# Kernel optimization log

Measured on AMD Instinct MI355X. Metric: run time of the kernel, lower is better.

## Reference

```python
import jax, jax.numpy as jnp
import numpy as np

EPS = 1e-6

def _phi(x):
    # ELU + 1 feature map: strictly positive
    return jax.nn.elu(x) + 1.0

def setup_inputs() -> dict:
    key = jax.random.key(0)
    kq, kk, kv = jax.random.split(key, 3)
    B, T, H, D = 4, 8192, 16, 64
    q = jax.random.normal(kq, (B, T, H, D), dtype=jnp.float32)
    k = jax.random.normal(kk, (B, T, H, D), dtype=jnp.float32)
    v = jax.random.normal(kv, (B, T, H, D), dtype=jnp.float32)
    return {"q": q, "k": k, "v": v}

def _linear_attention(q, k, v):
    # q,k,v: [B,T,H,D] -> out [B,T,H,D]
    phi_q = _phi(q)
    phi_k = _phi(k)
    # time-major for scan: [T,B,H,D]
    pq = jnp.moveaxis(phi_q, 1, 0)
    pk = jnp.moveaxis(phi_k, 1, 0)
    vv = jnp.moveaxis(v, 1, 0)
    B, H, D = pq.shape[1], pq.shape[2], pq.shape[3]
    S0 = jnp.zeros((B, H, D, D), dtype=q.dtype)
    z0 = jnp.zeros((B, H, D), dtype=q.dtype)

    def step(carry, inp):
        S, z = carry
        q_t, k_t, v_t = inp  # each [B,H,D]
        S = S + k_t[..., :, None] * v_t[..., None, :]  # [B,H,D,D]
        z = z + k_t
        num = jnp.einsum('bhd,bhde->bhe', q_t, S)
        den = jnp.einsum('bhd,bhd->bh', q_t, z) + EPS
        return (S, z), num / den[..., None]

    _, out = jax.lax.scan(step, (S0, z0), (pq, pk, vv))
    return jnp.moveaxis(out, 0, 1)  # [B,T,H,D]

def reference(q, k, v):
    return _linear_attention(q, k, v)
```

## Files before the change

kernel.cpp:

```cpp
#include <hip/hip_runtime.h>
#include <hip/hip_bf16.h>


#define EPS_ 1e-6f

constexpr int Bc  = 4;
constexpr int Tc  = 8192;
constexpr int Hc  = 16;
constexpr int Dc  = 64;
constexpr int CH  = 128;
constexpr int NCH = Tc / CH;
constexpr int BHc = Bc * Hc;
constexpr int REC = Dc * Dc + Dc;

typedef short  bf16x8 __attribute__((ext_vector_type(8)));
typedef float  f32x4  __attribute__((ext_vector_type(4)));

__device__ __forceinline__ float phi_f(float x) {
    return x > 0.f ? x + 1.f : __expf(x);
}
__device__ __forceinline__ unsigned short f2b(float x) {
    __hip_bfloat16 b = __float2bfloat16(x);
    return __builtin_bit_cast(unsigned short, b);
}
__device__ __forceinline__ float b2f(unsigned short u) {
    return __uint_as_float(((unsigned)u) << 16);
}

__global__ __launch_bounds__(256) void k_chunksum(const float* __restrict__ kin,
                                                  const float* __restrict__ vin,
                                                  float* __restrict__ ws) {
    const int chunk = blockIdx.x;
    const int bh = chunk >> 6, c = chunk & (NCH - 1);
    const int b  = bh >> 4,    h = bh & 15;
    const int t0 = c * CH;
    const int tid = threadIdx.x;

    __shared__ unsigned short ktr[64][136];
    __shared__ unsigned short vtr[64][136];
    __shared__ float zred[4][64];

    {
        const int c0 = (tid & 15) << 2;
        const int rl = ((tid >> 4) & 15) << 2;
        #pragma unroll
        for (int sh = 0; sh < 2; ++sh) {
            const int r0 = rl + sh * 64;
            unsigned short hk[4][4], hv[4][4];
            #pragma unroll
            for (int jj = 0; jj < 4; ++jj) {
                const size_t g = ((((size_t)b * Tc) + (t0 + r0 + jj)) * Hc + h) * Dc + c0;
                const float4 kk = *(const float4*)(kin + g);
                const float4 vv = *(const float4*)(vin + g);
                hk[jj][0] = f2b(phi_f(kk.x)); hk[jj][1] = f2b(phi_f(kk.y));
                hk[jj][2] = f2b(phi_f(kk.z)); hk[jj][3] = f2b(phi_f(kk.w));
                hv[jj][0] = f2b(vv.x); hv[jj][1] = f2b(vv.y);
                hv[jj][2] = f2b(vv.z); hv[jj][3] = f2b(vv.w);
            }
            #pragma unroll
            for (int j = 0; j < 4; ++j) {
                *(ushort4*)&ktr[c0 + j][r0] = make_ushort4(hk[0][j], hk[1][j], hk[2][j], hk[3][j]);
                *(ushort4*)&vtr[c0 + j][r0] = make_ushort4(hv[0][j], hv[1][j], hv[2][j], hv[3][j]);
            }
        }
    }
    __syncthreads();

    {
        const int d = tid & 63, part = tid >> 6;
        float zs = 0.f;
        #pragma unroll
        for (int j = 0; j < 4; j++) {
            bf16x8 kv = *(const bf16x8*)&ktr[d][part * 32 + j * 8];
            #pragma unroll
            for (int u = 0; u < 8; u++) zs += b2f((unsigned short)kv[u]);
        }
        zred[part][d] = zs;
    }

    const int w = tid >> 6, lane = tid & 63;
    const int l15 = lane & 15, quad = lane >> 4;
    f32x4 acc[4];
    #pragma unroll
    for (int nt = 0; nt < 4; nt++) acc[nt] = (f32x4){0.f, 0.f, 0.f, 0.f};
    #pragma unroll
    for (int ks = 0; ks < 4; ks++) {
        bf16x8 a = *(const bf16x8*)&vtr[16 * w + l15][quad * 8 + ks * 32];
        #pragma unroll
        for (int nt = 0; nt < 4; nt++) {
            bf16x8 bb = *(const bf16x8*)&ktr[16 * nt + l15][quad * 8 + ks * 32];
            acc[nt] = __builtin_amdgcn_mfma_f32_16x16x32_bf16(a, bb, acc[nt], 0, 0, 0);
        }
    }
    __syncthreads();

    float* rec = ws + (size_t)chunk * REC;
    #pragma unroll
    for (int nt = 0; nt < 4; nt++)
        #pragma unroll
        for (int r = 0; r < 4; r++) {
            const int e = 16 * w + quad * 4 + r;
            const int d = 16 * nt + l15;
            rec[e * 64 + d] = acc[nt][r];
        }
    if (tid < 64)
        rec[4096 + tid] = zred[0][tid] + zred[1][tid] + zred[2][tid] + zred[3][tid];
}

__global__ __launch_bounds__(256) void k_prefix(float* __restrict__ ws) {
    const int bh = blockIdx.x;
    const int e  = blockIdx.y * 256 + threadIdx.x;
    if (e >= REC) return;
    float* p = ws + (size_t)bh * NCH * REC + e;
    float run = 0.f;
    #pragma unroll 4
    for (int c = 0; c < NCH; ++c) {
        float x = p[(size_t)c * REC];
        p[(size_t)c * REC] = run;
        run += x;
    }
}

__global__ __launch_bounds__(512, 4) void k_output(const float* __restrict__ qin,
                                                   const float* __restrict__ kin,
                                                   const float* __restrict__ vin,
                                                   const float* __restrict__ ws,
                                                   float* __restrict__ outp) {
    const int chunk = blockIdx.x;
    const int bh = chunk >> 6, c = chunk & (NCH - 1);
    const int b = bh >> 4, h = bh & 15;
    const int t0 = c * CH;
    const int tid = threadIdx.x;
    const int w = tid >> 6, lane = tid & 63;
    const int l15 = lane & 15, quad = lane >> 4;

    __shared__ unsigned short qb[128][72];
    __shared__ unsigned short kb[128][72];
    __shared__ unsigned short sb[64][72];
    __shared__ unsigned short vb[64][136];
    __shared__ float zsh[64];
    __shared__ float den[128];

    {
        const int row = tid >> 2, cb = (tid & 3) << 4;
        const size_t g = ((((size_t)b * Tc) + (t0 + row)) * Hc + h) * Dc + cb;
        const float4* qp = (const float4*)(qin + g);
        const float4* kp = (const float4*)(kin + g);
        #pragma unroll
        for (int i = 0; i < 4; i++) {
            float4 qq = qp[i];
            float4 kk = kp[i];
            *(ushort4*)&qb[row][cb + 4 * i] =
                make_ushort4(f2b(phi_f(qq.x)), f2b(phi_f(qq.y)), f2b(phi_f(qq.z)), f2b(phi_f(qq.w)));
            *(ushort4*)&kb[row][cb + 4 * i] =
                make_ushort4(f2b(phi_f(kk.x)), f2b(phi_f(kk.y)), f2b(phi_f(kk.z)), f2b(phi_f(kk.w)));
        }
    }
    {
        const int c0 = (tid & 15) << 2;
        const int r0 = (tid >> 4) << 2;
        unsigned short hv[4][4];
        #pragma unroll
        for (int jj = 0; jj < 4; ++jj) {
            const size_t g = ((((size_t)b * Tc) + (t0 + r0 + jj)) * Hc + h) * Dc + c0;
            const float4 vv = *(const float4*)(vin + g);
            hv[jj][0] = f2b(vv.x); hv[jj][1] = f2b(vv.y);
            hv[jj][2] = f2b(vv.z); hv[jj][3] = f2b(vv.w);
        }
        #pragma unroll
        for (int j = 0; j < 4; ++j)
            *(ushort4*)&vb[c0 + j][r0] = make_ushort4(hv[0][j], hv[1][j], hv[2][j], hv[3][j]);
    }
    {
        const float* rec = ws + (size_t)chunk * REC;
        #pragma unroll
        for (int i = 0; i < 2; i++) {
            const int idx = tid + i * 512;
            float4 sv = ((const float4*)rec)[idx];
            const int flat = idx * 4, e = flat >> 6, d = flat & 63;
            *(ushort4*)&sb[e][d] = make_ushort4(f2b(sv.x), f2b(sv.y), f2b(sv.z), f2b(sv.w));
        }
        if (tid < 16) {
            float4 zv = ((const float4*)(rec + 4096))[tid];
            zsh[tid * 4 + 0] = zv.x; zsh[tid * 4 + 1] = zv.y;
            zsh[tid * 4 + 2] = zv.z; zsh[tid * 4 + 3] = zv.w;
        }
    }
    __syncthreads();

    if (tid < 128) {
        float s = 0.f;
        #pragma unroll
        for (int j = 0; j < 8; j++) {
            bf16x8 qv = *(const bf16x8*)&qb[tid][j * 8];
            #pragma unroll
            for (int u = 0; u < 8; u++) s += b2f((unsigned short)qv[u]) * zsh[j * 8 + u];
        }
        den[tid] = s + EPS_;
    }

    f32x4 acc[4];
    #pragma unroll
    for (int nt = 0; nt < 4; nt++) acc[nt] = (f32x4){0.f, 0.f, 0.f, 0.f};
    #pragma unroll
    for (int ks = 0; ks < 2; ks++) {
        bf16x8 a = *(const bf16x8*)&qb[16 * w + l15][quad * 8 + ks * 32];
        #pragma unroll
        for (int nt = 0; nt < 4; nt++) {
            bf16x8 bb = *(const bf16x8*)&sb[16 * nt + l15][quad * 8 + ks * 32];
            acc[nt] = __builtin_amdgcn_mfma_f32_16x16x32_bf16(a, bb, acc[nt], 0, 0, 0);
        }
    }

    f32x4 wt[8];
    #pragma unroll
    for (int nt = 0; nt < 8; nt++) wt[nt] = (f32x4){0.f, 0.f, 0.f, 0.f};
    #pragma unroll
    for (int ks = 0; ks < 2; ks++) {
        bf16x8 a = *(const bf16x8*)&qb[16 * w + l15][quad * 8 + ks * 32];
        #pragma unroll
        for (int nt = 0; nt < 4; nt++) {
            bf16x8 bb = *(const bf16x8*)&kb[16 * nt + l15][quad * 8 + ks * 32];
            wt[nt] = __builtin_amdgcn_mfma_f32_16x16x32_bf16(a, bb, wt[nt], 0, 0, 0);
        }
        if (w >= 4) {
            #pragma unroll
            for (int nt = 4; nt < 8; nt++) {
                bf16x8 bb = *(const bf16x8*)&kb[16 * nt + l15][quad * 8 + ks * 32];
                wt[nt] = __builtin_amdgcn_mfma_f32_16x16x32_bf16(a, bb, wt[nt], 0, 0, 0);
            }
        }
    }
    __syncthreads();

    {
        const int tbase = 16 * w + quad * 4;
        float rsum[4] = {0.f, 0.f, 0.f, 0.f};
        #pragma unroll
        for (int nt = 0; nt < 4; nt++) {
            const int s = 16 * nt + l15;
            #pragma unroll
            for (int r = 0; r < 4; r++) {
                float val = (s > tbase + r) ? 0.f : wt[nt][r];
                unsigned short wb16 = f2b(val);
                kb[tbase + r][s] = wb16;
                rsum[r] += b2f(wb16);
            }
        }
        if (w >= 4) {
            #pragma unroll
            for (int nt = 4; nt < 8; nt++) {
                const int s = 16 * nt + l15;
                #pragma unroll
                for (int r = 0; r < 4; r++) {
                    float val = (s > tbase + r) ? 0.f : wt[nt][r];
                    unsigned short wb16 = f2b(val);
                    qb[tbase + r][s - 64] = wb16;
                    rsum[r] += b2f(wb16);
                }
            }
        }
        #pragma unroll
        for (int r = 0; r < 4; r++) {
            float rs = rsum[r];
            rs += __shfl_xor(rs, 8, 16);
            rs += __shfl_xor(rs, 4, 16);
            rs += __shfl_xor(rs, 2, 16);
            rs += __shfl_xor(rs, 1, 16);
            if (l15 == 0) den[tbase + r] += rs;
        }
    }
    __syncthreads();

    #pragma unroll
    for (int ks = 0; ks < 2; ks++) {
        bf16x8 a = *(const bf16x8*)&kb[16 * w + l15][quad * 8 + ks * 32];
        #pragma unroll
        for (int nt = 0; nt < 4; nt++) {
            bf16x8 bb = *(const bf16x8*)&vb[16 * nt + l15][quad * 8 + ks * 32];
            acc[nt] = __builtin_amdgcn_mfma_f32_16x16x32_bf16(a, bb, acc[nt], 0, 0, 0);
        }
    }
    if (w >= 4) {
        #pragma unroll
        for (int ks = 2; ks < 4; ks++) {
            bf16x8 a = *(const bf16x8*)&qb[16 * w + l15][quad * 8 + (ks - 2) * 32];
            #pragma unroll
            for (int nt = 0; nt < 4; nt++) {
                bf16x8 bb = *(const bf16x8*)&vb[16 * nt + l15][quad * 8 + ks * 32];
                acc[nt] = __builtin_amdgcn_mfma_f32_16x16x32_bf16(a, bb, acc[nt], 0, 0, 0);
            }
        }
    }

    #pragma unroll
    for (int r = 0; r < 4; r++) {
        const int t = 16 * w + quad * 4 + r;
        const float inv = 1.0f / den[t];
        const size_t gbase = ((((size_t)b * Tc) + (t0 + t)) * Hc + h) * Dc;
        #pragma unroll
        for (int nt = 0; nt < 4; nt++) {
            outp[gbase + 16 * nt + l15] = acc[nt][r] * inv;
        }
    }
}

extern "C" void kernel_launch(void* const* d_in, const int* in_sizes, int n_in,
                              void* d_out, int out_size, void* d_ws, size_t ws_size,
                              hipStream_t stream) {
    const float* q = (const float*)d_in[0];
    const float* k = (const float*)d_in[1];
    const float* v = (const float*)d_in[2];
    float* out = (float*)d_out;
    float* ws  = (float*)d_ws;

    k_chunksum<<<BHc * NCH, 256, 0, stream>>>(k, v, ws);
    dim3 g2(BHc, (REC + 255) / 256);
    k_prefix<<<g2, 256, 0, stream>>>(ws);
    k_output<<<BHc * NCH, 512, 0, stream>>>(q, k, v, ws, out);
}
```

Measured before the change: 516.5 us.

## Replace per-chunk sum plus serial prefix with segmented in-block scan

The chunk-sum kernel now processes 4 consecutive chunks per block and keeps the running state in MFMA accumulators, writing exclusive prefixes inside each segment. A small kernel then scans only the 16 segment bases per head. The output kernel adds the segment base to the in-segment prefix. This is meant to remove the long serial 64-step prefix pass over the workspace, at the cost of fewer blocks in the first kernel and an extra base read per output block.

```diff
diff --git a/kernel.cpp b/kernel.cpp
--- a/kernel.cpp
+++ b/kernel.cpp
@@ -12,6 +12,8 @@
 constexpr int NCH = Tc / CH;
 constexpr int BHc = Bc * Hc;
 constexpr int REC = Dc * Dc + Dc;
+constexpr int SEG = 16;
+constexpr int CPS = NCH / SEG;
 
 typedef short  bf16x8 __attribute__((ext_vector_type(8)));
 typedef float  f32x4  __attribute__((ext_vector_type(4)));
@@ -27,98 +29,117 @@
     return __uint_as_float(((unsigned)u) << 16);
 }
 
-__global__ __launch_bounds__(256) void k_chunksum(const float* __restrict__ kin,
-                                                  const float* __restrict__ vin,
-                                                  float* __restrict__ ws) {
-    const int chunk = blockIdx.x;
-    const int bh = chunk >> 6, c = chunk & (NCH - 1);
-    const int b  = bh >> 4,    h = bh & 15;
-    const int t0 = c * CH;
+__global__ __launch_bounds__(256, 4) void k_chunkscan(const float* __restrict__ kin,
+                                                      const float* __restrict__ vin,
+                                                      float* __restrict__ ws) {
+    const int blk = blockIdx.x;
+    const int bh  = blk >> 4, seg = blk & (SEG - 1);
+    const int b   = bh >> 4,  h   = bh & 15;
     const int tid = threadIdx.x;
+    const int w = tid >> 6, lane = tid & 63;
+    const int l15 = lane & 15, quad = lane >> 4;
 
     __shared__ unsigned short ktr[64][136];
     __shared__ unsigned short vtr[64][136];
-    __shared__ float zred[4][64];
-
-    {
-        const int c0 = (tid & 15) << 2;
-        const int rl = ((tid >> 4) & 15) << 2;
+    __shared__ float zred[16][64];
+
+    const int c0 = (tid & 15) << 2;
+    const int rl = (tid >> 4) << 2;
+
+    f32x4 acc[4];
+    #pragma unroll
+    for (int nt = 0; nt < 4; nt++) acc[nt] = (f32x4){0.f, 0.f, 0.f, 0.f};
+    float zrun = 0.f;
+
+    for (int i = 0; i < CPS; ++i) {
+        const int c  = seg * CPS + i;
+        const int t0 = c * CH;
+
+        unsigned short hk[2][4][4], hv[2][4][4];
+        float zp[4] = {0.f, 0.f, 0.f, 0.f};
         #pragma unroll
         for (int sh = 0; sh < 2; ++sh) {
             const int r0 = rl + sh * 64;
-            unsigned short hk[4][4], hv[4][4];
             #pragma unroll
             for (int jj = 0; jj < 4; ++jj) {
                 const size_t g = ((((size_t)b * Tc) + (t0 + r0 + jj)) * Hc + h) * Dc + c0;
                 const float4 kk = *(const float4*)(kin + g);
                 const float4 vv = *(const float4*)(vin + g);
-                hk[jj][0] = f2b(phi_f(kk.x)); hk[jj][1] = f2b(phi_f(kk.y));
-                hk[jj][2] = f2b(phi_f(kk.z)); hk[jj][3] = f2b(phi_f(kk.w));
-                hv[jj][0] = f2b(vv.x); hv[jj][1] = f2b(vv.y);
-                hv[jj][2] = f2b(vv.z); hv[jj][3] = f2b(vv.w);
-            }
+                hk[sh][jj][0] = f2b(phi_f(kk.x)); hk[sh][jj][1] = f2b(phi_f(kk.y));
+                hk[sh][jj][2] = f2b(phi_f(kk.z)); hk[sh][jj][3] = f2b(phi_f(kk.w));
+                hv[sh][jj][0] = f2b(vv.x); hv[sh][jj][1] = f2b(vv.y);
+                hv[sh][jj][2] = f2b(vv.z); hv[sh][jj][3] = f2b(vv.w);
+                #pragma unroll
+                for (int j = 0; j < 4; ++j) zp[j] += b2f(hk[sh][jj][j]);
+            }
+        }
+        __syncthreads();
+
+        #pragma unroll
+        for (int sh = 0; sh < 2; ++sh) {
+            const int r0 = rl + sh * 64;
             #pragma unroll
             for (int j = 0; j < 4; ++j) {
-                *(ushort4*)&ktr[c0 + j][r0] = make_ushort4(hk[0][j], hk[1][j], hk[2][j], hk[3][j]);
-                *(ushort4*)&vtr[c0 + j][r0] = make_ushort4(hv[0][j], hv[1][j], hv[2][j], hv[3][j]);
-            }
-        }
-    }
-    __syncthreads();
-
-    {
-        const int d = tid & 63, part = tid >> 6;
-        float zs = 0.f;
-        #pragma unroll
-        for (int j = 0; j < 4; j++) {
-            bf16x8 kv = *(const bf16x8*)&ktr[d][part * 32 + j * 8];
-            #pragma unroll
-            for (int u = 0; u < 8; u++) zs += b2f((unsigned short)kv[u]);
-        }
-        zred[part][d] = zs;
-    }
-
-    const int w = tid >> 6, lane = tid & 63;
-    const int l15 = lane & 15, quad = lane >> 4;
-    f32x4 acc[4];
-    #pragma unroll
-    for (int nt = 0; nt < 4; nt++) acc[nt] = (f32x4){0.f, 0.f, 0.f, 0.f};
-    #pragma unroll
-    for (int ks = 0; ks < 4; ks++) {
-        bf16x8 a = *(const bf16x8*)&vtr[16 * w + l15][quad * 8 + ks * 32];
-        #pragma unroll
-        for (int nt = 0; nt < 4; nt++) {
-            bf16x8 bb = *(const bf16x8*)&ktr[16 * nt + l15][quad * 8 + ks * 32];
-            acc[nt] = __builtin_amdgcn_mfma_f32_16x16x32_bf16(a, bb, acc[nt], 0, 0, 0);
-        }
-    }
-    __syncthreads();
-
-    float* rec = ws + (size_t)chunk * REC;
-    #pragma unroll
-    for (int nt = 0; nt < 4; nt++)
-        #pragma unroll
-        for (int r = 0; r < 4; r++) {
-            const int e = 16 * w + quad * 4 + r;
-            const int d = 16 * nt + l15;
-            rec[e * 64 + d] = acc[nt][r];
-        }
-    if (tid < 64)
-        rec[4096 + tid] = zred[0][tid] + zred[1][tid] + zred[2][tid] + zred[3][tid];
-}
-
-__global__ __launch_bounds__(256) void k_prefix(float* __restrict__ ws) {
+                *(ushort4*)&ktr[c0 + j][r0] =
+                    make_ushort4(hk[sh][0][j], hk[sh][1][j], hk[sh][2][j], hk[sh][3][j]);
+                *(ushort4*)&vtr[c0 + j][r0] =
+                    make_ushort4(hv[sh][0][j], hv[sh][1][j], hv[sh][2][j], hv[sh][3][j]);
+            }
+        }
+        #pragma unroll
+        for (int j = 0; j < 4; ++j) zred[tid >> 4][c0 + j] = zp[j];
+
+        float* rec = ws + (size_t)(bh * NCH + c) * REC;
+        if (i > 0) {
+            #pragma unroll
+            for (int nt = 0; nt < 4; nt++)
+                #pragma unroll
+                for (int r = 0; r < 4; r++)
+                    rec[(16 * w + quad * 4 + r) * 64 + 16 * nt + l15] = acc[nt][r];
+        }
+        __syncthreads();
+
+        if (tid < 64) {
+            if (i > 0) rec[4096 + tid] = zrun;
+            float zs = 0.f;
+            #pragma unroll
+            for (int g = 0; g < 16; g++) zs += zred[g][tid];
+            zrun += zs;
+        }
+
+        #pragma unroll
+        for (int ks = 0; ks < 4; ks++) {
+            bf16x8 a = *(const bf16x8*)&vtr[16 * w + l15][quad * 8 + ks * 32];
+            #pragma unroll
+            for (int nt = 0; nt < 4; nt++) {
+                bf16x8 bb = *(const bf16x8*)&ktr[16 * nt + l15][quad * 8 + ks * 32];
+                acc[nt] = __builtin_amdgcn_mfma_f32_16x16x32_bf16(a, bb, acc[nt], 0, 0, 0);
+            }
+        }
+    }
+
+    {
+        float* rec0 = ws + (size_t)(bh * NCH + seg * CPS) * REC;
+        #pragma unroll
+        for (int nt = 0; nt < 4; nt++)
+            #pragma unroll
+            for (int r = 0; r < 4; r++)
+                rec0[(16 * w + quad * 4 + r) * 64 + 16 * nt + l15] = acc[nt][r];
+        if (tid < 64) rec0[4096 + tid] = zrun;
+    }
+}
+
+__global__ __launch_bounds__(256) void k_segscan(float* __restrict__ ws) {
     const int bh = blockIdx.x;
     const int e  = blockIdx.y * 256 + threadIdx.x;
     if (e >= REC) return;
     float* p = ws + (size_t)bh * NCH * REC + e;
+    float t[SEG];
+    #pragma unroll
+    for (int s = 0; s < SEG; ++s) t[s] = p[(size_t)(s * CPS) * REC];
     float run = 0.f;
-    #pragma unroll 4
-    for (int c = 0; c < NCH; ++c) {
-        float x = p[(size_t)c * REC];
-        p[(size_t)c * REC] = run;
-        run += x;
-    }
+    #pragma unroll
+    for (int s = 0; s < SEG; ++s) { p[(size_t)(s * CPS) * REC] = run; run += t[s]; }
 }
 
 __global__ __launch_bounds__(512, 4) void k_output(const float* __restrict__ qin,
@@ -173,17 +194,27 @@
     }
     {
         const float* rec = ws + (size_t)chunk * REC;
+        const float* bse = ws + (size_t)(bh * NCH + (c & ~(CPS - 1))) * REC;
+        const bool cz = ((c & (CPS - 1)) == 0);
         #pragma unroll
         for (int i = 0; i < 2; i++) {
             const int idx = tid + i * 512;
             float4 sv = ((const float4*)rec)[idx];
+            float4 bv = ((const float4*)bse)[idx];
+            float4 t;
+            if (cz) t = bv;
+            else { t.x = sv.x + bv.x; t.y = sv.y + bv.y; t.z = sv.z + bv.z; t.w = sv.w + bv.w; }
             const int flat = idx * 4, e = flat >> 6, d = flat & 63;
-            *(ushort4*)&sb[e][d] = make_ushort4(f2b(sv.x), f2b(sv.y), f2b(sv.z), f2b(sv.w));
+            *(ushort4*)&sb[e][d] = make_ushort4(f2b(t.x), f2b(t.y), f2b(t.z), f2b(t.w));
         }
         if (tid < 16) {
             float4 zv = ((const float4*)(rec + 4096))[tid];
-            zsh[tid * 4 + 0] = zv.x; zsh[tid * 4 + 1] = zv.y;
-            zsh[tid * 4 + 2] = zv.z; zsh[tid * 4 + 3] = zv.w;
+            float4 bz = ((const float4*)(bse + 4096))[tid];
+            float4 t;
+            if (cz) t = bz;
+            else { t.x = zv.x + bz.x; t.y = zv.y + bz.y; t.z = zv.z + bz.z; t.w = zv.w + bz.w; }
+            zsh[tid * 4 + 0] = t.x; zsh[tid * 4 + 1] = t.y;
+            zsh[tid * 4 + 2] = t.z; zsh[tid * 4 + 3] = t.w;
         }
     }
     __syncthreads();
@@ -314,8 +345,8 @@
     float* out = (float*)d_out;
     float* ws  = (float*)d_ws;
 
-    k_chunksum<<<BHc * NCH, 256, 0, stream>>>(k, v, ws);
+    k_chunkscan<<<BHc * SEG, 256, 0, stream>>>(k, v, ws);
     dim3 g2(BHc, (REC + 255) / 256);
-    k_prefix<<<g2, 256, 0, stream>>>(ws);
+    k_segscan<<<g2, 256, 0, stream>>>(ws);
     k_output<<<BHc * NCH, 512, 0, stream>>>(q, k, v, ws, out);
 }
```

New measurement: 501.3 us. 2.9% less time.
